# Performance work log

Measured on AMD Instinct MI355X. Metric: run time of the kernel, lower is better.

## Reference

```python
import jax, jax.numpy as jnp
import numpy as np

B, S, D, H, HD = 4, 2048, 2048, 16, 128
NEG_INF = -1e10


def setup_inputs() -> dict:
    key = jax.random.key(0)
    ks = jax.random.split(key, 7)
    scale = 1.0 / np.sqrt(D)  # variance_scaling(1.0, 'fan_in') approx
    inputs_q = jax.random.normal(ks[0], (B, S, D), jnp.float32)
    inputs_kv = jax.random.normal(ks[1], (B, S, D), jnp.float32)
    mask = jax.random.randint(ks[2], (B, 1, S, S), 0, 2, jnp.int32)
    Wq = jax.random.normal(ks[3], (D, H, HD), jnp.float32) * scale
    Wk = jax.random.normal(ks[4], (D, H, HD), jnp.float32) * scale
    Wv = jax.random.normal(ks[5], (D, H, HD), jnp.float32) * scale
    Wo = jax.random.normal(ks[6], (H, HD, D), jnp.float32) * (1.0 / np.sqrt(H * HD))
    return {"inputs_q": inputs_q, "inputs_kv": inputs_kv, "mask": mask,
            "Wq": Wq, "Wk": Wk, "Wv": Wv, "Wo": Wo}


def reference(inputs_q, inputs_kv, mask, Wq, Wk, Wv, Wo):
    # QKV projections: [B,S,D] x [D,H,HD] -> [B,S,H,HD]
    q = jnp.einsum('bsd,dhk->bshk', inputs_q, Wq)
    k = jnp.einsum('bsd,dhk->bshk', inputs_kv, Wk)
    v = jnp.einsum('bsd,dhk->bshk', inputs_kv, Wv)
    # mask -> additive bias: 0 where mask>0, else -1e10
    attn_bias = jnp.where(mask > 0, 0.0, NEG_INF).astype(q.dtype)  # [B,1,S,S]
    # scaled dot-product attention
    q = q / jnp.sqrt(jnp.asarray(HD, q.dtype))
    logits = jnp.einsum('bqhd,bkhd->bhqk', q, k) + attn_bias  # [B,H,S,S]
    weights = jax.nn.softmax(logits, axis=-1)
    x = jnp.einsum('bhqk,bkhd->bqhd', weights, v)  # [B,S,H,HD]
    # out projection contracts (heads, head_dim) -> embed
    out = jnp.einsum('bqhd,hdo->bqo', x, Wo)  # [B,S,D]
    return out
```

## Files before the change

kernel.cpp:

```cpp
#include <hip/hip_runtime.h>

typedef __attribute__((ext_vector_type(4))) float f32x4;
typedef __attribute__((ext_vector_type(8))) short bf16x8;
typedef __attribute__((ext_vector_type(4))) short bf16x4;
typedef unsigned int uint;
typedef unsigned short ushort;


__device__ __forceinline__ ushort f2bf(float f) {
  union { float f; uint u; } v; v.f = f;
  uint u = v.u;
  uint r = (u + 0x7FFFu + ((u >> 16) & 1u)) >> 16;
  return (ushort)r;
}
__device__ __forceinline__ float to_f32(float f) { return f; }
__device__ __forceinline__ float to_f32(ushort u) {
  union { uint u; float f; } v; v.u = ((uint)u) << 16;
  return v.f;
}

__device__ __forceinline__ uint cvt_pk_bf16(float lo, float hi) {
  uint r;
  asm("v_cvt_pk_bf16_f32 %0, %1, %2" : "=v"(r) : "v"(lo), "v"(hi));
  return r;
}

__device__ __forceinline__ float fexp2(float x) {
  float r;
  asm("v_exp_f32 %0, %1" : "=v"(r) : "v"(x));
  return r;
}

__device__ __forceinline__ f32x4 mfma16(bf16x4 a, bf16x4 b, f32x4 c) {
  asm("v_mfma_f32_16x16x16_bf16 %0, %1, %2, %0" : "+v"(c) : "v"(a), "v"(b));
  return c;
}

__device__ __forceinline__ void gload_lds16(const void* g, void* l) {
  __builtin_amdgcn_global_load_lds(
      (const __attribute__((address_space(1))) void*)g,
      (__attribute__((address_space(3))) void*)l, 16, 0, 0);
}


__global__ __launch_bounds__(256)
void conv_bf16(const float* __restrict__ in, ushort* __restrict__ out, long n) {
  long i = ((long)blockIdx.x * 256 + threadIdx.x) * 8;
  if (i >= n) return;
  float4 a = *(const float4*)(in + i);
  float4 b = *(const float4*)(in + i + 4);
  union { ushort u[8]; uint4 v; } o;
  o.u[0] = f2bf(a.x); o.u[1] = f2bf(a.y); o.u[2] = f2bf(a.z); o.u[3] = f2bf(a.w);
  o.u[4] = f2bf(b.x); o.u[5] = f2bf(b.y); o.u[6] = f2bf(b.z); o.u[7] = f2bf(b.w);
  *(uint4*)(out + i) = o.v;
}

template<typename T>
__global__ __launch_bounds__(256)
void transpose_to_bf16(const T* __restrict__ in, ushort* __restrict__ out, int R, int C) {
  __shared__ float tile[32][33];
  const size_t boff = (size_t)blockIdx.z * R * C;
  in += boff; out += boff;
  const int r0 = blockIdx.y * 32, c0 = blockIdx.x * 32;
  const int x = threadIdx.x, y = threadIdx.y;
#pragma unroll
  for (int j = 0; j < 32; j += 8)
    tile[y + j][x] = to_f32(in[(size_t)(r0 + y + j) * C + c0 + x]);
  __syncthreads();
#pragma unroll
  for (int j = 0; j < 32; j += 8)
    out[(size_t)(c0 + y + j) * R + r0 + x] = f2bf(tile[x][y + j]);
}

__global__ __launch_bounds__(256)
void pack_mask(const int* __restrict__ in, uint* __restrict__ out) {
  long t = (long)blockIdx.x * 256 + threadIdx.x;
  const int4* p = (const int4*)(in + t * 32);
  uint w = 0;
#pragma unroll
  for (int i = 0; i < 8; ++i) {
    int4 v = p[i];
    w |= (v.x > 0 ? 1u : 0u) << (i * 4 + 0);
    w |= (v.y > 0 ? 1u : 0u) << (i * 4 + 1);
    w |= (v.z > 0 ? 1u : 0u) << (i * 4 + 2);
    w |= (v.w > 0 ? 1u : 0u) << (i * 4 + 3);
  }
  out[t] = w;
}


template<int OUT_BF16>
__global__ __launch_bounds__(512, 2)
void gemm256(const ushort* __restrict__ A, const ushort* __restrict__ Bt,
             void* __restrict__ C, int M, int N, int K, float scale) {
  __shared__ ushort lA[2][256 * 64];
  __shared__ ushort lB[2][256 * 64];
  const int tid = threadIdx.x;
  const int wid = tid >> 6, lane = tid & 63;
  const int lg = lane >> 4, li = lane & 15;
  const int wm = wid >> 2, wn = wid & 3;
  const int m0 = blockIdx.y * 256, n0 = blockIdx.x * 256;

  int offA[4], offB[4];
#pragma unroll
  for (int i = 0; i < 4; ++i) {
    int off = i * 8192 + tid * 16;
    int row = off >> 7;
    int col = (off & 127) ^ ((row & 7) << 4);
    offA[i] = (m0 + row) * (K * 2) + col;
    offB[i] = (n0 + row) * (K * 2) + col;
  }
  const char* Ab = (const char*)A;
  const char* Bb = (const char*)Bt;

#define STAGE256(bufi, ktb)                                                   \
  do {                                                                        \
    _Pragma("unroll") for (int i = 0; i < 4; ++i)                             \
      gload_lds16(Ab + (size_t)(offA[i] + (ktb)),                             \
                  (char*)lA[bufi] + i * 8192 + wid * 1024);                   \
    _Pragma("unroll") for (int i = 0; i < 4; ++i)                             \
      gload_lds16(Bb + (size_t)(offB[i] + (ktb)),                             \
                  (char*)lB[bufi] + i * 8192 + wid * 1024);                   \
  } while (0)

  f32x4 acc[8][4] = {};
  const int NT = K >> 6;

  STAGE256(0, 0);

  for (int t = 0; t < NT; ++t) {
    const int cur = t & 1;
    if (t > 0) __builtin_amdgcn_s_barrier();
    if (t + 1 < NT) {
      STAGE256(cur ^ 1, (t + 1) * 128);
      asm volatile("s_waitcnt vmcnt(8)" ::: "memory");
    } else {
      asm volatile("s_waitcnt vmcnt(0)" ::: "memory");
    }
    __builtin_amdgcn_s_barrier();
    __builtin_amdgcn_sched_barrier(0);

    const char* la = (const char*)lA[cur];
    const char* lb = (const char*)lB[cur];
    bf16x8 afr[4][2];
#pragma unroll
    for (int q = 0; q < 4; ++q) {
      const int mh = q >> 1;
      const int nh = (q == 1 || q == 2) ? 1 : 0;
      if ((q & 1) == 0) {
#pragma unroll
        for (int mi = 0; mi < 4; ++mi)
#pragma unroll
          for (int ks = 0; ks < 2; ++ks) {
            const int row = wm * 128 + (mh * 4 + mi) * 16 + li;
            afr[mi][ks] = *(const bf16x8*)(
                la + row * 128 + ((ks * 64 + lg * 16) ^ ((li & 7) << 4)));
          }
      }
      bf16x8 bfr[2][2];
#pragma unroll
      for (int ni = 0; ni < 2; ++ni)
#pragma unroll
        for (int ks = 0; ks < 2; ++ks) {
          const int row = wn * 64 + (nh * 2 + ni) * 16 + li;
          bfr[ni][ks] = *(const bf16x8*)(
              lb + row * 128 + ((ks * 64 + lg * 16) ^ ((li & 7) << 4)));
        }
      __builtin_amdgcn_s_setprio(1);
#pragma unroll
      for (int ks = 0; ks < 2; ++ks)
#pragma unroll
        for (int mi = 0; mi < 4; ++mi)
#pragma unroll
          for (int ni = 0; ni < 2; ++ni)
            acc[mh * 4 + mi][nh * 2 + ni] = __builtin_amdgcn_mfma_f32_16x16x32_bf16(
                afr[mi][ks], bfr[ni][ks], acc[mh * 4 + mi][nh * 2 + ni], 0, 0, 0);
      __builtin_amdgcn_s_setprio(0);
    }
  }
#undef STAGE256

  const int r0 = m0 + wm * 128 + lg * 4;
  const int c0 = n0 + wn * 64 + li;
#pragma unroll
  for (int mi = 0; mi < 8; ++mi)
#pragma unroll
    for (int ni = 0; ni < 4; ++ni)
#pragma unroll
      for (int r = 0; r < 4; ++r) {
        size_t idx = (size_t)(r0 + mi * 16 + r) * N + (c0 + ni * 16);
        float v = acc[mi][ni][r] * scale;
        if (OUT_BF16) ((ushort*)C)[idx] = f2bf(v);
        else          ((float*)C)[idx]  = v;
      }
}


__global__ __launch_bounds__(256, 2)
void flash_attn5(const ushort* __restrict__ Q, const ushort* __restrict__ K,
                 const ushort* __restrict__ VT, const uint* __restrict__ maskp,
                 ushort* __restrict__ X) {
  __shared__ ushort lK[2][64 * 128];
  __shared__ ushort lVT[2][128 * 64];

  const int tid = threadIdx.x;
  const int wid = tid >> 6;
  const int lane = tid & 63;
  const int lg = lane >> 4, li = lane & 15;

  const int flat = blockIdx.x;
  const int xcd = flat & 7;
  const int j = flat >> 3;
  const int bh = xcd * 8 + (j >> 4);
  const int qt = j & 15;
  const int b = bh >> 4, h = bh & 15;
  const int q0 = qt * 128;
  const int qbase = q0 + wid * 32;

  bf16x8 bq[2][4];
#pragma unroll
  for (int g = 0; g < 2; ++g) {
    const ushort* qrow = Q + (size_t)(b * 2048 + qbase + g * 16 + li) * 2048 + h * 128;
#pragma unroll
    for (int kk = 0; kk < 4; ++kk)
      bq[g][kk] = *(const bf16x8*)(qrow + kk * 32 + lg * 8);
  }

  const uint* mqb[2] = {
      maskp + (size_t)(b * 2048 + qbase + li) * 64,
      maskp + (size_t)(b * 2048 + qbase + 16 + li) * 64};
  uint2 wcur[2] = {*(const uint2*)mqb[0], *(const uint2*)mqb[1]};

  f32x4 acc_o[2][8] = {};
  f32x4 acc_l[2] = {};
  float m[2] = {-3e38f, -3e38f};

  const bf16x4 vone = {(short)0x3F80, (short)0x3F80, (short)0x3F80, (short)0x3F80};

  const char* gk[4];
  const char* gv[4];
#pragma unroll
  for (int i = 0; i < 4; ++i) {
    int fl = i * 4096 + tid * 16;
    int rowK = fl >> 8;
    int colK = (fl & 255) ^ ((rowK & 15) << 4);
    gk[i] = (const char*)K + ((size_t)(b * 2048 + rowK) * 2048 + h * 128) * 2 + colK;
    int rowV = fl >> 7;
    int colV = (fl & 127) ^ ((rowV & 7) << 4);
    gv[i] = (const char*)VT + ((size_t)((b * 16 + h) * 128 + rowV) * 2048) * 2 + colV;
  }

#define FSTAGE(bufi)                                                          \
  do {                                                                        \
    _Pragma("unroll") for (int i = 0; i < 4; ++i)                             \
      gload_lds16(gk[i], (char*)lK[bufi] + i * 4096 + wid * 1024);            \
    _Pragma("unroll") for (int i = 0; i < 4; ++i)                             \
      gload_lds16(gv[i], (char*)lVT[bufi] + i * 4096 + wid * 1024);           \
    _Pragma("unroll") for (int i = 0; i < 4; ++i) {                           \
      gk[i] += 262144; gv[i] += 128;                                          \
    }                                                                         \
  } while (0)

  FSTAGE(0);

  for (int it = 0; it < 32; ++it) {
    const int cur = it & 1;
    if (it > 0) __builtin_amdgcn_s_barrier();
    uint2 wn[2];
    if (it < 31) {
      FSTAGE(cur ^ 1);
      wn[0] = *(const uint2*)(mqb[0] + (it + 1) * 2);
      wn[1] = *(const uint2*)(mqb[1] + (it + 1) * 2);
      asm volatile("s_waitcnt vmcnt(10)" ::: "memory");
    } else {
      asm volatile("s_waitcnt vmcnt(0)" ::: "memory");
    }
    __builtin_amdgcn_s_barrier();
    __builtin_amdgcn_sched_barrier(0);

    const char* lk = (const char*)lK[cur];
    const char* lv = (const char*)lVT[cur];

    f32x4 accs[2][4] = {};
#pragma unroll
    for (int kk = 0; kk < 4; ++kk)
#pragma unroll
      for (int n = 0; n < 4; ++n) {
        bf16x8 ak = *(const bf16x8*)(lk + (n * 16 + li) * 256 +
                                     ((kk * 64 + lg * 16) ^ (li << 4)));
        accs[0][n] = __builtin_amdgcn_mfma_f32_16x16x32_bf16(ak, bq[0][kk], accs[0][n], 0, 0, 0);
        accs[1][n] = __builtin_amdgcn_mfma_f32_16x16x32_bf16(ak, bq[1][kk], accs[1][n], 0, 0, 0);
      }

    uint pkg[2][8];
#pragma unroll
    for (int g = 0; g < 2; ++g) {
      float sv[16];
      float pmax = -3e38f;
#pragma unroll
      for (int n = 0; n < 4; ++n) {
        uint w = (n < 2) ? wcur[g].x : wcur[g].y;
#pragma unroll
        for (int r = 0; r < 4; ++r) {
          int bit = (n & 1) * 16 + lg * 4 + r;
          float s = ((w >> bit) & 1u) ? accs[g][n][r] : -1e10f;
          sv[n * 4 + r] = s;
          pmax = fmaxf(pmax, s);
        }
      }
      pmax = fmaxf(pmax, __shfl_xor(pmax, 16, 64));
      pmax = fmaxf(pmax, __shfl_xor(pmax, 32, 64));

      if (!__all(pmax - m[g] <= 11.5f)) {
        float mnew = fmaxf(m[g], pmax);
        float alpha = fexp2(m[g] - mnew);
#pragma unroll
        for (int r = 0; r < 4; ++r) acc_l[g][r] *= alpha;
#pragma unroll
        for (int f = 0; f < 8; ++f)
#pragma unroll
          for (int r = 0; r < 4; ++r) acc_o[g][f][r] *= alpha;
        m[g] = mnew;
      }

#pragma unroll
      for (int i = 0; i < 8; ++i) {
        float p0 = fexp2(sv[2 * i] - m[g]);
        float p1 = fexp2(sv[2 * i + 1] - m[g]);
        pkg[g][i] = cvt_pk_bf16(p0, p1);
      }
    }

#pragma unroll
    for (int n = 0; n < 4; ++n) {
      union { uint u[2]; bf16x4 v; } b0, b1;
      b0.u[0] = pkg[0][2 * n]; b0.u[1] = pkg[0][2 * n + 1];
      b1.u[0] = pkg[1][2 * n]; b1.u[1] = pkg[1][2 * n + 1];
      acc_l[0] = mfma16(vone, b0.v, acc_l[0]);
      acc_l[1] = mfma16(vone, b1.v, acc_l[1]);
#pragma unroll
      for (int f = 0; f < 8; ++f) {
        bf16x4 av = *(const bf16x4*)(lv + (f * 16 + li) * 128 +
                                     ((n * 32 + lg * 8) ^ ((li & 7) << 4)));
        acc_o[0][f] = mfma16(av, b0.v, acc_o[0][f]);
        acc_o[1][f] = mfma16(av, b1.v, acc_o[1][f]);
      }
    }

    if (it < 31) { wcur[0] = wn[0]; wcur[1] = wn[1]; }
  }
#undef FSTAGE

  asm volatile("s_nop 7\n\ts_nop 7\n\ts_nop 7" ::: "memory");

#pragma unroll
  for (int g = 0; g < 2; ++g) {
    const float inv_l = 1.0f / acc_l[g][0];
    ushort* xrow = X + (size_t)(b * 2048 + qbase + g * 16 + li) * 2048 + h * 128;
#pragma unroll
    for (int f = 0; f < 8; ++f) {
      union { ushort u[4]; uint2 v; } o;
#pragma unroll
      for (int r = 0; r < 4; ++r) o.u[r] = f2bf(acc_o[g][f][r] * inv_l);
      *(uint2*)(xrow + f * 16 + lg * 4) = o.v;
    }
  }
}


extern "C" void kernel_launch(void* const* d_in, const int* in_sizes, int n_in,
                              void* d_out, int out_size, void* d_ws, size_t ws_size,
                              hipStream_t stream) {
  const float* inputs_q  = (const float*)d_in[0];
  const float* inputs_kv = (const float*)d_in[1];
  const int*   mask      = (const int*)d_in[2];
  const float* Wq        = (const float*)d_in[3];
  const float* Wk        = (const float*)d_in[4];
  const float* Wv        = (const float*)d_in[5];
  const float* Wo        = (const float*)d_in[6];
  float* out = (float*)d_out;
  char* ws = (char*)d_ws;

  uint*   maskp = (uint*)(ws + 0);
  ushort* xq    = (ushort*)(ws + 2097152);
  ushort* xkv   = (ushort*)(ws + 35651584);
  ushort* WqT   = (ushort*)(ws + 69206016);
  ushort* WkT   = (ushort*)(ws + 77594624);
  ushort* WvT   = (ushort*)(ws + 85983232);
  ushort* WoT   = (ushort*)(ws + 94371840);
  ushort* Qb    = (ushort*)(ws + 102760448);
  ushort* Kb    = (ushort*)(ws + 136314880);
  ushort* Vb    = (ushort*)(ws + 169869312);
  ushort* VTb   = xq;
  ushort* Xb    = xkv;

  const long NE = 8192L * 2048;
  conv_bf16<<<8192, 256, 0, stream>>>(inputs_q,  xq,  NE);
  conv_bf16<<<8192, 256, 0, stream>>>(inputs_kv, xkv, NE);

  dim3 tb(32, 8);
  transpose_to_bf16<float><<<dim3(64, 64, 1), tb, 0, stream>>>(Wq, WqT, 2048, 2048);
  transpose_to_bf16<float><<<dim3(64, 64, 1), tb, 0, stream>>>(Wk, WkT, 2048, 2048);
  transpose_to_bf16<float><<<dim3(64, 64, 1), tb, 0, stream>>>(Wv, WvT, 2048, 2048);
  transpose_to_bf16<float><<<dim3(64, 64, 1), tb, 0, stream>>>(Wo, WoT, 2048, 2048);

  pack_mask<<<2048, 256, 0, stream>>>(mask, maskp);

  const float qscale = 0.12751744504593677f;
  gemm256<1><<<dim3(8, 32), 512, 0, stream>>>(xq,  WqT, Qb, 8192, 2048, 2048, qscale);
  gemm256<1><<<dim3(8, 32), 512, 0, stream>>>(xkv, WkT, Kb, 8192, 2048, 2048, 1.0f);
  gemm256<1><<<dim3(8, 32), 512, 0, stream>>>(xkv, WvT, Vb, 8192, 2048, 2048, 1.0f);

  transpose_to_bf16<ushort><<<dim3(64, 64, 4), tb, 0, stream>>>(Vb, VTb, 2048, 2048);

  flash_attn5<<<1024, 256, 0, stream>>>(Qb, Kb, VTb, maskp, Xb);

  gemm256<0><<<dim3(8, 32), 512, 0, stream>>>(Xb, WoT, out, 8192, 2048, 2048, 1.0f);
}
```

Measured before the change: 610.5 us.

## Route softmax probabilities through LDS to use 16x16x32 MFMA for PV

The flash attention kernel now writes the packed bf16 probabilities of each wave into a per-wave LDS tile and reads them back in the 8-element K layout. This lets the P·V and row-sum products use the 16x16x32 bf16 MFMA instead of twice as many 16x16x16 inline-asm MFMAs. The change also raises wave priority around the MFMA blocks, unrolls the main loop by two and drops the trailing nops. The cost is an extra LDS write and read round trip per iteration plus 16 KB more shared memory, which could reduce occupancy.

```diff
diff --git a/kernel.cpp b/kernel.cpp
--- a/kernel.cpp
+++ b/kernel.cpp
@@ -2,9 +2,10 @@
 
 typedef __attribute__((ext_vector_type(4))) float f32x4;
 typedef __attribute__((ext_vector_type(8))) short bf16x8;
-typedef __attribute__((ext_vector_type(4))) short bf16x4;
 typedef unsigned int uint;
 typedef unsigned short ushort;
+
+#define mfma32 __builtin_amdgcn_mfma_f32_16x16x32_bf16
 
 
 __device__ __forceinline__ ushort f2bf(float f) {
@@ -29,11 +30,6 @@
   float r;
   asm("v_exp_f32 %0, %1" : "=v"(r) : "v"(x));
   return r;
-}
-
-__device__ __forceinline__ f32x4 mfma16(bf16x4 a, bf16x4 b, f32x4 c) {
-  asm("v_mfma_f32_16x16x16_bf16 %0, %1, %2, %0" : "+v"(c) : "v"(a), "v"(b));
-  return c;
 }
 
 __device__ __forceinline__ void gload_lds16(const void* g, void* l) {
@@ -173,7 +169,7 @@
         for (int mi = 0; mi < 4; ++mi)
 #pragma unroll
           for (int ni = 0; ni < 2; ++ni)
-            acc[mh * 4 + mi][nh * 2 + ni] = __builtin_amdgcn_mfma_f32_16x16x32_bf16(
+            acc[mh * 4 + mi][nh * 2 + ni] = mfma32(
                 afr[mi][ks], bfr[ni][ks], acc[mh * 4 + mi][nh * 2 + ni], 0, 0, 0);
       __builtin_amdgcn_s_setprio(0);
     }
@@ -197,11 +193,12 @@
 
 
 __global__ __launch_bounds__(256, 2)
-void flash_attn5(const ushort* __restrict__ Q, const ushort* __restrict__ K,
+void flash_attn6(const ushort* __restrict__ Q, const ushort* __restrict__ K,
                  const ushort* __restrict__ VT, const uint* __restrict__ maskp,
                  ushort* __restrict__ X) {
   __shared__ ushort lK[2][64 * 128];
   __shared__ ushort lVT[2][128 * 64];
+  __shared__ ushort lP[4][2][16 * 64];
 
   const int tid = threadIdx.x;
   const int wid = tid >> 6;
@@ -235,7 +232,8 @@
   f32x4 acc_l[2] = {};
   float m[2] = {-3e38f, -3e38f};
 
-  const bf16x4 vone = {(short)0x3F80, (short)0x3F80, (short)0x3F80, (short)0x3F80};
+  const short ob = (short)0x3F80;
+  const bf16x8 vone8 = {ob, ob, ob, ob, ob, ob, ob, ob};
 
   const char* gk[4];
   const char* gv[4];
@@ -263,6 +261,10 @@
 
   FSTAGE(0);
 
+  ushort* lp0 = lP[wid][0];
+  ushort* lp1 = lP[wid][1];
+
+#pragma unroll 2
   for (int it = 0; it < 32; ++it) {
     const int cur = it & 1;
     if (it > 0) __builtin_amdgcn_s_barrier();
@@ -282,17 +284,18 @@
     const char* lv = (const char*)lVT[cur];
 
     f32x4 accs[2][4] = {};
+    __builtin_amdgcn_s_setprio(1);
 #pragma unroll
     for (int kk = 0; kk < 4; ++kk)
 #pragma unroll
       for (int n = 0; n < 4; ++n) {
         bf16x8 ak = *(const bf16x8*)(lk + (n * 16 + li) * 256 +
                                      ((kk * 64 + lg * 16) ^ (li << 4)));
-        accs[0][n] = __builtin_amdgcn_mfma_f32_16x16x32_bf16(ak, bq[0][kk], accs[0][n], 0, 0, 0);
-        accs[1][n] = __builtin_amdgcn_mfma_f32_16x16x32_bf16(ak, bq[1][kk], accs[1][n], 0, 0, 0);
-      }
-
-    uint pkg[2][8];
+        accs[0][n] = mfma32(ak, bq[0][kk], accs[0][n], 0, 0, 0);
+        accs[1][n] = mfma32(ak, bq[1][kk], accs[1][n], 0, 0, 0);
+      }
+    __builtin_amdgcn_s_setprio(0);
+
 #pragma unroll
     for (int g = 0; g < 2; ++g) {
       float sv[16];
@@ -323,35 +326,44 @@
         m[g] = mnew;
       }
 
+      uint pk[8];
 #pragma unroll
       for (int i = 0; i < 8; ++i) {
         float p0 = fexp2(sv[2 * i] - m[g]);
         float p1 = fexp2(sv[2 * i + 1] - m[g]);
-        pkg[g][i] = cvt_pk_bf16(p0, p1);
-      }
-    }
-
-#pragma unroll
-    for (int n = 0; n < 4; ++n) {
-      union { uint u[2]; bf16x4 v; } b0, b1;
-      b0.u[0] = pkg[0][2 * n]; b0.u[1] = pkg[0][2 * n + 1];
-      b1.u[0] = pkg[1][2 * n]; b1.u[1] = pkg[1][2 * n + 1];
-      acc_l[0] = mfma16(vone, b0.v, acc_l[0]);
-      acc_l[1] = mfma16(vone, b1.v, acc_l[1]);
+        pk[i] = cvt_pk_bf16(p0, p1);
+      }
+
+      ushort* lpg = g ? lp1 : lp0;
+#pragma unroll
+      for (int n = 0; n < 4; ++n) {
+        uint2 pw; pw.x = pk[2 * n]; pw.y = pk[2 * n + 1];
+        *(uint2*)((char*)lpg + li * 128 + ((n * 32 + lg * 8) ^ ((li & 7) << 4))) = pw;
+      }
+    }
+
+    __builtin_amdgcn_s_setprio(1);
+#pragma unroll
+    for (int kc = 0; kc < 2; ++kc) {
+      bf16x8 bp0 = *(const bf16x8*)((const char*)lp0 + li * 128 +
+                                    ((kc * 64 + lg * 16) ^ ((li & 7) << 4)));
+      bf16x8 bp1 = *(const bf16x8*)((const char*)lp1 + li * 128 +
+                                    ((kc * 64 + lg * 16) ^ ((li & 7) << 4)));
+      acc_l[0] = mfma32(vone8, bp0, acc_l[0], 0, 0, 0);
+      acc_l[1] = mfma32(vone8, bp1, acc_l[1], 0, 0, 0);
 #pragma unroll
       for (int f = 0; f < 8; ++f) {
-        bf16x4 av = *(const bf16x4*)(lv + (f * 16 + li) * 128 +
-                                     ((n * 32 + lg * 8) ^ ((li & 7) << 4)));
-        acc_o[0][f] = mfma16(av, b0.v, acc_o[0][f]);
-        acc_o[1][f] = mfma16(av, b1.v, acc_o[1][f]);
-      }
-    }
+        bf16x8 av = *(const bf16x8*)(lv + (f * 16 + li) * 128 +
+                                     ((kc * 64 + lg * 16) ^ ((li & 7) << 4)));
+        acc_o[0][f] = mfma32(av, bp0, acc_o[0][f], 0, 0, 0);
+        acc_o[1][f] = mfma32(av, bp1, acc_o[1][f], 0, 0, 0);
+      }
+    }
+    __builtin_amdgcn_s_setprio(0);
 
     if (it < 31) { wcur[0] = wn[0]; wcur[1] = wn[1]; }
   }
 #undef FSTAGE
-
-  asm volatile("s_nop 7\n\ts_nop 7\n\ts_nop 7" ::: "memory");
 
 #pragma unroll
   for (int g = 0; g < 2; ++g) {
@@ -413,7 +425,7 @@
 
   transpose_to_bf16<ushort><<<dim3(64, 64, 4), tb, 0, stream>>>(Vb, VTb, 2048, 2048);
 
-  flash_attn5<<<1024, 256, 0, stream>>>(Qb, Kb, VTb, maskp, Xb);
+  flash_attn6<<<1024, 256, 0, stream>>>(Qb, Kb, VTb, maskp, Xb);
 
   gemm256<0><<<dim3(8, 32), 512, 0, stream>>>(Xb, WoT, out, 8192, 2048, 2048, 1.0f);
 }
```

Measured after the change: 593.1 us. 1.03x faster.
